# Kernel tuning notes

Hardware: AMD Instinct MI355X
Metric: run time of the kernel (lower is better)

## Reference

```python
import jax, jax.numpy as jnp
import numpy as np

TOPK = 13
ALPHA = 1.0
BETA = 6.0
CENTER_RADIUS = 0.5
EPS = 1e-7
IMG = 2048
STRIDES = (8, 16, 32)


def _make_anchor_points():
    pts = []
    for s in STRIDES:
        n = IMG // s
        c = (jnp.arange(n, dtype=jnp.float32) + 0.5) * s
        yy, xx = jnp.meshgrid(c, c, indexing='ij')
        pts.append(jnp.stack([xx.ravel(), yy.ravel()], axis=-1))
    return jnp.concatenate(pts, axis=0)  # [86016, 2]


def setup_inputs() -> dict:
    key = jax.random.key(0)
    k = jax.random.split(key, 6)
    anchor_points = _make_anchor_points()           # [P, 2]
    P = anchor_points.shape[0]
    C, G = 365, 100
    pred_scores = jax.random.normal(k[0], (P, C), dtype=jnp.float32) * 2.0 - 2.0
    pred_objectness = jax.random.normal(k[1], (P,), dtype=jnp.float32)
    # predicted boxes: anchor +- positive ltrb distances (valid xyxy)
    dist = jax.random.uniform(k[2], (P, 4), minval=2.0, maxval=120.0, dtype=jnp.float32)
    pred_boxes = jnp.concatenate([anchor_points - dist[:, :2], anchor_points + dist[:, 2:]], axis=-1)
    ctr = jax.random.uniform(k[3], (G, 2), minval=64.0, maxval=IMG - 64.0, dtype=jnp.float32)
    half = jax.random.uniform(k[4], (G, 2), minval=16.0, maxval=160.0, dtype=jnp.float32)
    gt_boxes = jnp.concatenate([ctr - half, ctr + half], axis=-1)  # [G, 4] xyxy
    gt_labels = jax.random.randint(k[5], (G,), 0, C, dtype=jnp.int64)
    valid_class_mask = jnp.ones((C,), dtype=bool)
    return {
        'pred_scores': pred_scores,
        'pred_boxes': pred_boxes,
        'pred_objectness': pred_objectness,
        'anchor_points': anchor_points,
        'gt_boxes': gt_boxes,
        'gt_labels': gt_labels,
        'valid_class_mask': valid_class_mask,
    }


def _iou_matrix(gt_boxes, pred_boxes):
    # gt: [G,4], pred: [P,4] -> [G,P]
    lt = jnp.maximum(gt_boxes[:, None, :2], pred_boxes[None, :, :2])
    rb = jnp.minimum(gt_boxes[:, None, 2:], pred_boxes[None, :, 2:])
    wh = jnp.clip(rb - lt, 0.0)
    inter = wh[..., 0] * wh[..., 1]
    area_g = jnp.prod(jnp.clip(gt_boxes[:, 2:] - gt_boxes[:, :2], 0.0), axis=-1)
    area_p = jnp.prod(jnp.clip(pred_boxes[:, 2:] - pred_boxes[:, :2], 0.0), axis=-1)
    union = area_g[:, None] + area_p[None, :] - inter
    return inter / (union + EPS)


def reference(pred_scores, pred_boxes, pred_objectness, anchor_points, gt_boxes, gt_labels, valid_class_mask):
    P, C = pred_scores.shape
    G = gt_boxes.shape[0]
    gt_labels = gt_labels.astype(jnp.int32)

    valid_gt = (gt_labels >= 0) & (gt_labels < C) & valid_class_mask[jnp.clip(gt_labels, 0, C - 1)]

    # inside-box mask [G, P]
    ax, ay = anchor_points[:, 0], anchor_points[:, 1]
    inside = ((ax[None, :] >= gt_boxes[:, 0:1]) & (ax[None, :] <= gt_boxes[:, 2:3]) &
              (ay[None, :] >= gt_boxes[:, 1:2]) & (ay[None, :] <= gt_boxes[:, 3:4]))

    gt_center = (gt_boxes[:, :2] + gt_boxes[:, 2:]) * 0.5               # [G,2]
    half_size = jnp.clip((gt_boxes[:, 2:] - gt_boxes[:, :2]) * 0.5, 1.0)
    center_delta = jnp.abs(anchor_points[None, :, :] - gt_center[:, None, :]) / half_size[:, None, :]  # [G,P,2]
    cd_max = center_delta.max(axis=-1)                                   # [G,P]
    center_mask = cd_max <= CENTER_RADIUS

    strict = inside & center_mask
    has_center = strict.any(axis=1, keepdims=True)                       # [G,1]
    cand = jnp.where(has_center, strict, inside)                         # fallback to inside-only

    iou = _iou_matrix(gt_boxes, pred_boxes)                              # [G,P]
    cls_scores = jax.nn.sigmoid(pred_scores[:, jnp.clip(gt_labels, 0, C - 1)].T)  # [G,P]
    pred_obj = jax.nn.sigmoid(pred_objectness)                           # [P]
    quality = jnp.sqrt(jnp.clip(pred_obj[None, :] * cls_scores, 0.0))
    center_prior = jnp.exp(-0.5 * jnp.sum(center_delta ** 2, axis=-1))   # [G,P]
    align = (quality ** ALPHA) * (iou ** BETA) * center_prior            # [G,P], >= 0

    masked = jnp.where(cand & valid_gt[:, None], align, -1.0)
    top_val, top_idx = jax.lax.top_k(masked, TOPK)                       # [G,TOPK]
    # scatter per-GT top-k back to [G,P]; entries with value -1 (non-candidates) stay excluded
    sel = jnp.full((G, P), -1.0, dtype=align.dtype)
    sel = sel.at[jnp.arange(G)[:, None], top_idx].set(jnp.where(top_val > -0.5, top_val, -1.0))

    # sequential 'override only if strictly greater' == per-point argmax with ties to earliest GT
    metric = sel.max(axis=0)                                             # [P]
    best_gt = jnp.argmax(sel, axis=0)                                    # [P]
    fg_mask = metric > -0.5

    overlap = iou[best_gt, jnp.arange(P)]                                # [P]
    matched_gt_indices = jnp.where(fg_mask, best_gt, -1)
    matched_labels = jnp.where(fg_mask, gt_labels[best_gt], -1)

    target_boxes = jnp.where(fg_mask[:, None], gt_boxes[best_gt], 0.0)   # [P,4]
    lab_idx = jnp.clip(matched_labels, 0, C - 1)
    score_val = jnp.where(fg_mask, jnp.clip(overlap, 0.1), 0.0)
    target_scores = jnp.zeros((P, C), dtype=pred_scores.dtype).at[jnp.arange(P), lab_idx].set(score_val)

    return (target_scores, target_boxes, fg_mask, matched_gt_indices, matched_labels)
```

## Files before the change

### kernel.cpp

```cpp
#include <hip/hip_runtime.h>
#include <cstdint>
#include <cstddef>

#define TOPK 13
#define MAXC 2560
#define NITER 10
#define NLEV 3
#define FILL_F4 1024

__global__ __launch_bounds__(256) void pdl_zero_topk_kernel(
    const float*  __restrict__ scores,
    const float4* __restrict__ pboxes,
    const float*  __restrict__ obj,
    const float4* __restrict__ gtb,
    const int*    __restrict__ glab,
    const unsigned char* __restrict__ vmask,
    unsigned long long* __restrict__ ws_keys,
    float* __restrict__ out,
    int C, int G, long long nfloat4)
{
    const int bid = blockIdx.x;
    const int tid = threadIdx.x;

    if (bid >= G) {
        float4* dst = (float4*)out;
        const float4 z = make_float4(0.0f, 0.0f, 0.0f, 0.0f);
        const long long s0 = (long long)(bid - G) * FILL_F4;
        const long long i = s0 + tid;
        if (i       < nfloat4) dst[i]       = z;
        if (i + 256 < nfloat4) dst[i + 256] = z;
        if (i + 512 < nfloat4) dst[i + 512] = z;
        if (i + 768 < nfloat4) dst[i + 768] = z;
        return;
    }

    const int g = bid;
    if (tid < TOPK) ws_keys[g * TOPK + tid] = 0ULL;

    const float4 gb = gtb[g];
    const int lab = glab[g];
    bool valid = (lab >= 0) && (lab < C);
    if (valid) {
        valid = (vmask[lab] != 0) || (vmask[4 * (size_t)lab] != 0) ||
                (vmask[8 * (size_t)lab] != 0);
    }
    if (!valid) return;

    __shared__ int s_flag;
    __shared__ unsigned long long s_merge[4 * TOPK];

    if (tid == 0) s_flag = 0;

    const float cx = (gb.x + gb.z) * 0.5f;
    const float cy = (gb.y + gb.w) * 0.5f;
    const float hx = fmaxf((gb.z - gb.x) * 0.5f, 1.0f);
    const float hy = fmaxf((gb.w - gb.y) * 0.5f, 1.0f);
    const float area_g = fmaxf(gb.z - gb.x, 0.0f) * fmaxf(gb.w - gb.y, 0.0f);

    const int ls[NLEV]   = {8, 16, 32};
    const int ln[NLEV]   = {256, 128, 64};
    const int loff[NLEV] = {0, 65536, 81920};
    int x0[NLEV], y0[NLEV], ww[NLEV], cnt[NLEV];
    int T = 0;
    #pragma unroll
    for (int l = 0; l < NLEV; ++l) {
        const float fs = (float)ls[l];
        int xa = (int)floorf(gb.x / fs - 0.5f);
        int xb = (int)ceilf (gb.z / fs - 0.5f);
        int ya = (int)floorf(gb.y / fs - 0.5f);
        int yb = (int)ceilf (gb.w / fs - 0.5f);
        xa = xa > 0 ? xa : 0;
        ya = ya > 0 ? ya : 0;
        xb = xb < ln[l] - 1 ? xb : ln[l] - 1;
        yb = yb < ln[l] - 1 ? yb : ln[l] - 1;
        int w = xb - xa + 1; if (w < 0) w = 0;
        int h = yb - ya + 1; if (h < 0) h = 0;
        x0[l] = xa; y0[l] = ya; ww[l] = w;
        cnt[l] = w * h;
        T += cnt[l];
    }
    __syncthreads();

    const int lane = tid & 63;
    const int wid  = tid >> 6;

    bool any_strict = false;
    for (int j = tid; j < T; j += 256) {
        int jj = j, l = 0;
        if (jj >= cnt[0]) { jj -= cnt[0]; l = 1; if (jj >= cnt[1]) { jj -= cnt[1]; l = 2; } }
        const int iy = jj / ww[l];
        const int ix = jj - iy * ww[l];
        const float fs = (float)ls[l];
        const float ax = ((float)(x0[l] + ix) + 0.5f) * fs;
        const float ay = ((float)(y0[l] + iy) + 0.5f) * fs;
        if (ax >= gb.x && ax <= gb.z && ay >= gb.y && ay <= gb.w) {
            const float cdx = fabsf(ax - cx) / hx;
            const float cdy = fabsf(ay - cy) / hy;
            if (fmaxf(cdx, cdy) <= 0.5f) any_strict = true;
        }
    }
    if (any_strict) s_flag = 1;
    __syncthreads();
    const bool has_center = (s_flag != 0);

    unsigned long long k[NITER];
    #pragma unroll
    for (int it = 0; it < NITER; ++it) {
        k[it] = 0ULL;
        const int j = tid + (it << 8);
        if (j >= T) continue;
        int jj = j, l = 0;
        if (jj >= cnt[0]) { jj -= cnt[0]; l = 1; if (jj >= cnt[1]) { jj -= cnt[1]; l = 2; } }
        const int iy = jj / ww[l];
        const int ix = jj - iy * ww[l];
        const float fs = (float)ls[l];
        const float ax = ((float)(x0[l] + ix) + 0.5f) * fs;
        const float ay = ((float)(y0[l] + iy) + 0.5f) * fs;
        if (!(ax >= gb.x && ax <= gb.z && ay >= gb.y && ay <= gb.w)) continue;
        const float cdx = fabsf(ax - cx) / hx;
        const float cdy = fabsf(ay - cy) / hy;
        const bool strict = fmaxf(cdx, cdy) <= 0.5f;
        if (has_center && !strict) continue;

        const int p = loff[l] + (y0[l] + iy) * ln[l] + (x0[l] + ix);
        const float4 pb = pboxes[p];
        const float so = 1.0f / (1.0f + expf(-obj[p]));
        const float sc = 1.0f / (1.0f + expf(-scores[(size_t)p * C + lab]));
        const float prior = expf(-0.5f * (cdx * cdx + cdy * cdy));
        const float ltx = fmaxf(gb.x, pb.x);
        const float lty = fmaxf(gb.y, pb.y);
        const float rbx = fminf(gb.z, pb.z);
        const float rby = fminf(gb.w, pb.w);
        const float wi = fmaxf(rbx - ltx, 0.0f);
        const float hi = fmaxf(rby - lty, 0.0f);
        const float inter = wi * hi;
        const float area_p = fmaxf(pb.z - pb.x, 0.0f) * fmaxf(pb.w - pb.y, 0.0f);
        const float iou = inter / (area_g + area_p - inter + 1e-7f);
        const float q = sqrtf(fmaxf(so * sc, 0.0f));
        const float i2 = iou * iou;
        const float align = q * (i2 * i2 * i2) * prior;

        k[it] = ((unsigned long long)__float_as_uint(align) << 32)
              | (unsigned long long)(0xFFFFFFFFu ^ (unsigned)p);
    }

    {
        unsigned long long W = ~0ULL;
        for (int r = 0; r < TOPK; ++r) {
            unsigned long long loc = 0ULL;
            #pragma unroll
            for (int it = 0; it < NITER; ++it)
                if (k[it] < W && k[it] > loc) loc = k[it];
            unsigned long long wb = loc;
            #pragma unroll
            for (int d = 32; d >= 1; d >>= 1) {
                const unsigned long long o = __shfl_xor(wb, d, 64);
                if (o > wb) wb = o;
            }
            if (lane == 0) s_merge[wid * TOPK + r] = wb;
            W = wb;
        }
    }
    __syncthreads();

    if (wid == 0) {
        const unsigned long long v =
            (lane < 4 * TOPK) ? s_merge[lane] : 0ULL;
        unsigned long long W = ~0ULL;
        for (int r = 0; r < TOPK; ++r) {
            unsigned long long wb = (v < W) ? v : 0ULL;
            #pragma unroll
            for (int d = 32; d >= 1; d >>= 1) {
                const unsigned long long o = __shfl_xor(wb, d, 64);
                if (o > wb) wb = o;
            }
            if (lane == 0) ws_keys[g * TOPK + r] = wb;
            W = wb;
        }
    }
}

__global__ __launch_bounds__(256) void pdl_finalize_kernel(
    const float4* __restrict__ pboxes,
    const float4* __restrict__ gtb,
    const int*    __restrict__ glab,
    const unsigned long long* __restrict__ ws_keys,
    float* __restrict__ out,
    int P, int C, int G)
{
    const int tid = threadIdx.x;
    const int p0  = blockIdx.x * 256;
    const int p   = p0 + tid;

    __shared__ unsigned long long s_best[256];
    s_best[tid] = 0ULL;
    __syncthreads();

    const int npairs = G * TOPK;
    for (int j = tid; j < npairs; j += 256) {
        const unsigned long long k = ws_keys[j];
        if (k == 0ULL) continue;
        const unsigned pp = 0xFFFFFFFFu ^ (unsigned)(k & 0xFFFFFFFFull);
        const int d = (int)pp - p0;
        if (d >= 0 && d < 256) {
            const int g = j / TOPK;
            const unsigned long long key2 =
                (k & 0xFFFFFFFF00000000ull) |
                (unsigned long long)(0xFFFFFFFFu - (unsigned)g);
            atomicMax(&s_best[d], key2);
        }
    }
    __syncthreads();

    if (p < P) {
        const unsigned long long k = s_best[tid];
        const bool fg = (k != 0ULL);
        float4 tb = make_float4(0.0f, 0.0f, 0.0f, 0.0f);
        float mgi = -1.0f, mlab = -1.0f;
        if (fg) {
            const int bg = (int)(0xFFFFFFFFu - (unsigned)(k & 0xFFFFFFFFull));
            const float4 gbx = gtb[bg];
            const float4 pb  = pboxes[p];
            const float ltx = fmaxf(gbx.x, pb.x);
            const float lty = fmaxf(gbx.y, pb.y);
            const float rbx = fminf(gbx.z, pb.z);
            const float rby = fminf(gbx.w, pb.w);
            const float wi = fmaxf(rbx - ltx, 0.0f);
            const float hi = fmaxf(rby - lty, 0.0f);
            const float inter = wi * hi;
            const float ag = fmaxf(gbx.z - gbx.x, 0.0f) * fmaxf(gbx.w - gbx.y, 0.0f);
            const float ap = fmaxf(pb.z - pb.x, 0.0f) * fmaxf(pb.w - pb.y, 0.0f);
            const float iou = inter / (ag + ap - inter + 1e-7f);
            const int lb = glab[bg];
            tb   = gbx;
            mgi  = (float)bg;
            mlab = (float)lb;
            int lbc = lb < 0 ? 0 : (lb > C - 1 ? C - 1 : lb);
            out[(size_t)p * C + lbc] = fmaxf(iou, 0.1f);
        }
        float4* boxes_out = (float4*)(out + (size_t)P * C);
        boxes_out[p] = tb;
        const size_t base = (size_t)P * C + (size_t)4 * P;
        out[base + p]                 = fg ? 1.0f : 0.0f;
        out[base + (size_t)P + p]     = mgi;
        out[base + (size_t)2 * P + p] = mlab;
    }
}

extern "C" void kernel_launch(void* const* d_in, const int* in_sizes, int n_in,
                              void* d_out, int out_size, void* d_ws, size_t ws_size,
                              hipStream_t stream)
{
    (void)n_in; (void)out_size; (void)ws_size;

    const float*  scores = (const float*)d_in[0];
    const float4* pboxes = (const float4*)d_in[1];
    const float*  obj    = (const float*)d_in[2];
    const float4* gtb    = (const float4*)d_in[4];
    const int*    glab   = (const int*)d_in[5];
    const unsigned char* vmask = (const unsigned char*)d_in[6];

    const int P = in_sizes[2];
    const int C = in_sizes[0] / P;
    const int G = in_sizes[5];

    unsigned long long* ws_keys = (unsigned long long*)d_ws;
    float* out = (float*)d_out;

    const long long nfloat4 = ((long long)P * C) / 4;
    const int NZB = (int)((nfloat4 + FILL_F4 - 1) / FILL_F4);

    pdl_zero_topk_kernel<<<G + NZB, 256, 0, stream>>>(scores, pboxes, obj, gtb,
                                                      glab, vmask, ws_keys, out,
                                                      C, G, nfloat4);
    pdl_finalize_kernel<<<(P + 255) / 256, 256, 0, stream>>>(pboxes, gtb, glab,
                                                             ws_keys, out, P, C, G);
}
```

Baseline: 36.46 us.

## Split pipeline into topk, zero-fill+small-outputs, and sparse scatter kernels

Moves the large zero-fill of the score tensor out of the top-k kernel and into a second kernel that also writes the per-point boxes, mask, index and label outputs. A third kernel then recomputes the per-point best GT and scatters only the IoU score values. The aim is to keep the top-k blocks from competing with the heavy zero-fill blocks, so the G top-k blocks finish sooner. The cost is an extra launch and a second pass over the workspace keys, and the zero-fill now runs after top-k instead of overlapping with it.

```diff
diff --git a/kernel.cpp b/kernel.cpp
--- a/kernel.cpp
+++ b/kernel.cpp
@@ -8,7 +8,7 @@
 #define NLEV 3
 #define FILL_F4 1024
 
-__global__ __launch_bounds__(256) void pdl_zero_topk_kernel(
+__global__ __launch_bounds__(256) void pdl_topk_kernel(
     const float*  __restrict__ scores,
     const float4* __restrict__ pboxes,
     const float*  __restrict__ obj,
@@ -16,25 +16,11 @@
     const int*    __restrict__ glab,
     const unsigned char* __restrict__ vmask,
     unsigned long long* __restrict__ ws_keys,
-    float* __restrict__ out,
-    int C, int G, long long nfloat4)
+    int C)
 {
-    const int bid = blockIdx.x;
+    const int g   = blockIdx.x;
     const int tid = threadIdx.x;
 
-    if (bid >= G) {
-        float4* dst = (float4*)out;
-        const float4 z = make_float4(0.0f, 0.0f, 0.0f, 0.0f);
-        const long long s0 = (long long)(bid - G) * FILL_F4;
-        const long long i = s0 + tid;
-        if (i       < nfloat4) dst[i]       = z;
-        if (i + 256 < nfloat4) dst[i + 256] = z;
-        if (i + 512 < nfloat4) dst[i + 512] = z;
-        if (i + 768 < nfloat4) dst[i + 768] = z;
-        return;
-    }
-
-    const int g = bid;
     if (tid < TOPK) ws_keys[g * TOPK + tid] = 0ULL;
 
     const float4 gb = gtb[g];
@@ -180,17 +166,29 @@
     }
 }
 
-__global__ __launch_bounds__(256) void pdl_finalize_kernel(
-    const float4* __restrict__ pboxes,
+__global__ __launch_bounds__(256) void pdl_fill_outputs_kernel(
     const float4* __restrict__ gtb,
     const int*    __restrict__ glab,
     const unsigned long long* __restrict__ ws_keys,
     float* __restrict__ out,
-    int P, int C, int G)
+    int P, int C, int G, long long nfloat4, int ACB)
 {
+    const int bid = blockIdx.x;
     const int tid = threadIdx.x;
-    const int p0  = blockIdx.x * 256;
-    const int p   = p0 + tid;
+
+    if (bid >= ACB) {
+        float4* dst = (float4*)out;
+        const float4 z = make_float4(0.0f, 0.0f, 0.0f, 0.0f);
+        const long long i = (long long)(bid - ACB) * FILL_F4 + tid;
+        if (i       < nfloat4) dst[i]       = z;
+        if (i + 256 < nfloat4) dst[i + 256] = z;
+        if (i + 512 < nfloat4) dst[i + 512] = z;
+        if (i + 768 < nfloat4) dst[i + 768] = z;
+        return;
+    }
+
+    const int p0 = bid * 256;
+    const int p  = p0 + tid;
 
     __shared__ unsigned long long s_best[256];
     s_best[tid] = 0ULL;
@@ -218,6 +216,55 @@
         float4 tb = make_float4(0.0f, 0.0f, 0.0f, 0.0f);
         float mgi = -1.0f, mlab = -1.0f;
         if (fg) {
+            const int bg = (int)(0xFFFFFFFFu - (unsigned)(k & 0xFFFFFFFFull));
+            tb   = gtb[bg];
+            mgi  = (float)bg;
+            mlab = (float)glab[bg];
+        }
+        float4* boxes_out = (float4*)(out + (size_t)P * C);
+        boxes_out[p] = tb;
+        const size_t base = (size_t)P * C + (size_t)4 * P;
+        out[base + p]                 = fg ? 1.0f : 0.0f;
+        out[base + (size_t)P + p]     = mgi;
+        out[base + (size_t)2 * P + p] = mlab;
+    }
+}
+
+__global__ __launch_bounds__(256) void pdl_scatter_kernel(
+    const float4* __restrict__ pboxes,
+    const float4* __restrict__ gtb,
+    const int*    __restrict__ glab,
+    const unsigned long long* __restrict__ ws_keys,
+    float* __restrict__ out,
+    int P, int C, int G)
+{
+    const int tid = threadIdx.x;
+    const int p0  = blockIdx.x * 256;
+    const int p   = p0 + tid;
+
+    __shared__ unsigned long long s_best[256];
+    s_best[tid] = 0ULL;
+    __syncthreads();
+
+    const int npairs = G * TOPK;
+    for (int j = tid; j < npairs; j += 256) {
+        const unsigned long long k = ws_keys[j];
+        if (k == 0ULL) continue;
+        const unsigned pp = 0xFFFFFFFFu ^ (unsigned)(k & 0xFFFFFFFFull);
+        const int d = (int)pp - p0;
+        if (d >= 0 && d < 256) {
+            const int g = j / TOPK;
+            const unsigned long long key2 =
+                (k & 0xFFFFFFFF00000000ull) |
+                (unsigned long long)(0xFFFFFFFFu - (unsigned)g);
+            atomicMax(&s_best[d], key2);
+        }
+    }
+    __syncthreads();
+
+    if (p < P) {
+        const unsigned long long k = s_best[tid];
+        if (k != 0ULL) {
             const int bg = (int)(0xFFFFFFFFu - (unsigned)(k & 0xFFFFFFFFull));
             const float4 gbx = gtb[bg];
             const float4 pb  = pboxes[p];
@@ -231,19 +278,10 @@
             const float ag = fmaxf(gbx.z - gbx.x, 0.0f) * fmaxf(gbx.w - gbx.y, 0.0f);
             const float ap = fmaxf(pb.z - pb.x, 0.0f) * fmaxf(pb.w - pb.y, 0.0f);
             const float iou = inter / (ag + ap - inter + 1e-7f);
-            const int lb = glab[bg];
-            tb   = gbx;
-            mgi  = (float)bg;
-            mlab = (float)lb;
-            int lbc = lb < 0 ? 0 : (lb > C - 1 ? C - 1 : lb);
-            out[(size_t)p * C + lbc] = fmaxf(iou, 0.1f);
-        }
-        float4* boxes_out = (float4*)(out + (size_t)P * C);
-        boxes_out[p] = tb;
-        const size_t base = (size_t)P * C + (size_t)4 * P;
-        out[base + p]                 = fg ? 1.0f : 0.0f;
-        out[base + (size_t)P + p]     = mgi;
-        out[base + (size_t)2 * P + p] = mlab;
+            int lb = glab[bg];
+            lb = lb < 0 ? 0 : (lb > C - 1 ? C - 1 : lb);
+            out[(size_t)p * C + lb] = fmaxf(iou, 0.1f);
+        }
     }
 }
 
@@ -269,10 +307,13 @@
 
     const long long nfloat4 = ((long long)P * C) / 4;
     const int NZB = (int)((nfloat4 + FILL_F4 - 1) / FILL_F4);
-
-    pdl_zero_topk_kernel<<<G + NZB, 256, 0, stream>>>(scores, pboxes, obj, gtb,
-                                                      glab, vmask, ws_keys, out,
-                                                      C, G, nfloat4);
-    pdl_finalize_kernel<<<(P + 255) / 256, 256, 0, stream>>>(pboxes, gtb, glab,
-                                                             ws_keys, out, P, C, G);
+    const int ACB = (P + 255) / 256;
+
+    pdl_topk_kernel<<<G, 256, 0, stream>>>(scores, pboxes, obj, gtb, glab,
+                                           vmask, ws_keys, C);
+    pdl_fill_outputs_kernel<<<ACB + NZB, 256, 0, stream>>>(gtb, glab, ws_keys,
+                                                           out, P, C, G,
+                                                           nfloat4, ACB);
+    pdl_scatter_kernel<<<ACB, 256, 0, stream>>>(pboxes, gtb, glab, ws_keys,
+                                                out, P, C, G);
 }
```

Result: slower. 46.60 us (+27.8%).

## Fuse top-k and finalize kernels into one with a global completion counter

Applied to the files above, without the earlier changes.

The producer top-k blocks and the zero-fill/finalize work now live in one launch. Consumer blocks own 96-row slices: they zero their slice of target_scores, spin-wait on a global done counter until all G producer blocks have published their keys, then scatter and finalize their rows. This removes the second kernel launch and the gap between the two kernels, and it overlaps the zero-fill with the top-k work. In exchange it adds a memset launch for the counter and a spin-wait that assumes producer blocks get scheduled before consumers occupy all slots. It also makes every consumer block rescan all G*TOPK keys for a much smaller row range.

```diff
diff --git a/kernel.cpp b/kernel.cpp
--- a/kernel.cpp
+++ b/kernel.cpp
@@ -3,222 +3,233 @@
 #include <cstddef>
 
 #define TOPK 13
-#define MAXC 2560
 #define NITER 10
 #define NLEV 3
-#define FILL_F4 1024
-
-__global__ __launch_bounds__(256) void pdl_zero_topk_kernel(
+#define ROWS 96
+
+__global__ __launch_bounds__(256, 4) void pdl_mega_kernel(
     const float*  __restrict__ scores,
     const float4* __restrict__ pboxes,
     const float*  __restrict__ obj,
     const float4* __restrict__ gtb,
     const int*    __restrict__ glab,
     const unsigned char* __restrict__ vmask,
+    unsigned int* __restrict__ done,
     unsigned long long* __restrict__ ws_keys,
     float* __restrict__ out,
-    int C, int G, long long nfloat4)
+    int P, int C, int G)
 {
     const int bid = blockIdx.x;
     const int tid = threadIdx.x;
-
-    if (bid >= G) {
+    const int lane = tid & 63;
+    const int wid  = tid >> 6;
+
+    __shared__ int s_flag;
+    __shared__ unsigned long long s_merge[4 * TOPK];
+    __shared__ unsigned long long s_best[ROWS];
+
+    if (bid < G) {
+        const int g = bid;
+        if (tid < TOPK) ws_keys[g * TOPK + tid] = 0ULL;
+
+        const float4 gb = gtb[g];
+        const int lab = glab[g];
+        bool valid = (lab >= 0) && (lab < C);
+        if (valid) {
+            valid = (vmask[lab] != 0) || (vmask[4 * (size_t)lab] != 0) ||
+                    (vmask[8 * (size_t)lab] != 0);
+        }
+        if (valid) {
+            if (tid == 0) s_flag = 0;
+
+            const float cx = (gb.x + gb.z) * 0.5f;
+            const float cy = (gb.y + gb.w) * 0.5f;
+            const float hx = fmaxf((gb.z - gb.x) * 0.5f, 1.0f);
+            const float hy = fmaxf((gb.w - gb.y) * 0.5f, 1.0f);
+            const float area_g = fmaxf(gb.z - gb.x, 0.0f) * fmaxf(gb.w - gb.y, 0.0f);
+
+            const int ls[NLEV]   = {8, 16, 32};
+            const int ln[NLEV]   = {256, 128, 64};
+            const int loff[NLEV] = {0, 65536, 81920};
+            int x0[NLEV], y0[NLEV], ww[NLEV], cnt[NLEV];
+            int T = 0;
+            #pragma unroll
+            for (int l = 0; l < NLEV; ++l) {
+                const float fs = (float)ls[l];
+                int xa = (int)floorf(gb.x / fs - 0.5f);
+                int xb = (int)ceilf (gb.z / fs - 0.5f);
+                int ya = (int)floorf(gb.y / fs - 0.5f);
+                int yb = (int)ceilf (gb.w / fs - 0.5f);
+                xa = xa > 0 ? xa : 0;
+                ya = ya > 0 ? ya : 0;
+                xb = xb < ln[l] - 1 ? xb : ln[l] - 1;
+                yb = yb < ln[l] - 1 ? yb : ln[l] - 1;
+                int w = xb - xa + 1; if (w < 0) w = 0;
+                int h = yb - ya + 1; if (h < 0) h = 0;
+                x0[l] = xa; y0[l] = ya; ww[l] = w;
+                cnt[l] = w * h;
+                T += cnt[l];
+            }
+            __syncthreads();
+
+            bool any_strict = false;
+            for (int j = tid; j < T; j += 256) {
+                int jj = j, l = 0;
+                if (jj >= cnt[0]) { jj -= cnt[0]; l = 1; if (jj >= cnt[1]) { jj -= cnt[1]; l = 2; } }
+                const int iy = jj / ww[l];
+                const int ix = jj - iy * ww[l];
+                const float fs = (float)ls[l];
+                const float ax = ((float)(x0[l] + ix) + 0.5f) * fs;
+                const float ay = ((float)(y0[l] + iy) + 0.5f) * fs;
+                if (ax >= gb.x && ax <= gb.z && ay >= gb.y && ay <= gb.w) {
+                    const float cdx = fabsf(ax - cx) / hx;
+                    const float cdy = fabsf(ay - cy) / hy;
+                    if (fmaxf(cdx, cdy) <= 0.5f) any_strict = true;
+                }
+            }
+            if (any_strict) s_flag = 1;
+            __syncthreads();
+            const bool has_center = (s_flag != 0);
+
+            unsigned long long k[NITER];
+            #pragma unroll
+            for (int it = 0; it < NITER; ++it) {
+                k[it] = 0ULL;
+                const int j = tid + (it << 8);
+                if (j >= T) continue;
+                int jj = j, l = 0;
+                if (jj >= cnt[0]) { jj -= cnt[0]; l = 1; if (jj >= cnt[1]) { jj -= cnt[1]; l = 2; } }
+                const int iy = jj / ww[l];
+                const int ix = jj - iy * ww[l];
+                const float fs = (float)ls[l];
+                const float ax = ((float)(x0[l] + ix) + 0.5f) * fs;
+                const float ay = ((float)(y0[l] + iy) + 0.5f) * fs;
+                if (!(ax >= gb.x && ax <= gb.z && ay >= gb.y && ay <= gb.w)) continue;
+                const float cdx = fabsf(ax - cx) / hx;
+                const float cdy = fabsf(ay - cy) / hy;
+                const bool strict = fmaxf(cdx, cdy) <= 0.5f;
+                if (has_center && !strict) continue;
+
+                const int p = loff[l] + (y0[l] + iy) * ln[l] + (x0[l] + ix);
+                const float4 pb = pboxes[p];
+                const float so = 1.0f / (1.0f + expf(-obj[p]));
+                const float sc = 1.0f / (1.0f + expf(-scores[(size_t)p * C + lab]));
+                const float prior = expf(-0.5f * (cdx * cdx + cdy * cdy));
+                const float ltx = fmaxf(gb.x, pb.x);
+                const float lty = fmaxf(gb.y, pb.y);
+                const float rbx = fminf(gb.z, pb.z);
+                const float rby = fminf(gb.w, pb.w);
+                const float wi = fmaxf(rbx - ltx, 0.0f);
+                const float hi = fmaxf(rby - lty, 0.0f);
+                const float inter = wi * hi;
+                const float area_p = fmaxf(pb.z - pb.x, 0.0f) * fmaxf(pb.w - pb.y, 0.0f);
+                const float iou = inter / (area_g + area_p - inter + 1e-7f);
+                const float q = sqrtf(fmaxf(so * sc, 0.0f));
+                const float i2 = iou * iou;
+                const float align = q * (i2 * i2 * i2) * prior;
+
+                k[it] = ((unsigned long long)__float_as_uint(align) << 32)
+                      | (unsigned long long)(0xFFFFFFFFu ^ (unsigned)p);
+            }
+
+            {
+                unsigned long long W = ~0ULL;
+                for (int r = 0; r < TOPK; ++r) {
+                    unsigned long long loc = 0ULL;
+                    #pragma unroll
+                    for (int it = 0; it < NITER; ++it)
+                        if (k[it] < W && k[it] > loc) loc = k[it];
+                    unsigned long long wb = loc;
+                    #pragma unroll
+                    for (int d = 32; d >= 1; d >>= 1) {
+                        const unsigned long long o = __shfl_xor(wb, d, 64);
+                        if (o > wb) wb = o;
+                    }
+                    if (lane == 0) s_merge[wid * TOPK + r] = wb;
+                    W = wb;
+                }
+            }
+            __syncthreads();
+
+            if (wid == 0) {
+                const unsigned long long v =
+                    (lane < 4 * TOPK) ? s_merge[lane] : 0ULL;
+                unsigned long long W = ~0ULL;
+                for (int r = 0; r < TOPK; ++r) {
+                    unsigned long long wb = (v < W) ? v : 0ULL;
+                    #pragma unroll
+                    for (int d = 32; d >= 1; d >>= 1) {
+                        const unsigned long long o = __shfl_xor(wb, d, 64);
+                        if (o > wb) wb = o;
+                    }
+                    if (lane == 0) ws_keys[g * TOPK + r] = wb;
+                    W = wb;
+                }
+            }
+        }
+        __syncthreads();
+        if (tid == 0) {
+            __threadfence();
+            atomicAdd(done, 1u);
+        }
+        return;
+    }
+
+    const int cb = bid - G;
+    const int a0 = cb * ROWS;
+    int a1 = a0 + ROWS; if (a1 > P) a1 = P;
+    const int na = a1 - a0;
+    if (na <= 0) return;
+
+    for (int i = tid; i < na; i += 256) s_best[i] = 0ULL;
+
+    {
         float4* dst = (float4*)out;
         const float4 z = make_float4(0.0f, 0.0f, 0.0f, 0.0f);
-        const long long s0 = (long long)(bid - G) * FILL_F4;
-        const long long i = s0 + tid;
-        if (i       < nfloat4) dst[i]       = z;
-        if (i + 256 < nfloat4) dst[i + 256] = z;
-        if (i + 512 < nfloat4) dst[i + 512] = z;
-        if (i + 768 < nfloat4) dst[i + 768] = z;
-        return;
-    }
-
-    const int g = bid;
-    if (tid < TOPK) ws_keys[g * TOPK + tid] = 0ULL;
-
-    const float4 gb = gtb[g];
-    const int lab = glab[g];
-    bool valid = (lab >= 0) && (lab < C);
-    if (valid) {
-        valid = (vmask[lab] != 0) || (vmask[4 * (size_t)lab] != 0) ||
-                (vmask[8 * (size_t)lab] != 0);
-    }
-    if (!valid) return;
-
-    __shared__ int s_flag;
-    __shared__ unsigned long long s_merge[4 * TOPK];
-
-    if (tid == 0) s_flag = 0;
-
-    const float cx = (gb.x + gb.z) * 0.5f;
-    const float cy = (gb.y + gb.w) * 0.5f;
-    const float hx = fmaxf((gb.z - gb.x) * 0.5f, 1.0f);
-    const float hy = fmaxf((gb.w - gb.y) * 0.5f, 1.0f);
-    const float area_g = fmaxf(gb.z - gb.x, 0.0f) * fmaxf(gb.w - gb.y, 0.0f);
-
-    const int ls[NLEV]   = {8, 16, 32};
-    const int ln[NLEV]   = {256, 128, 64};
-    const int loff[NLEV] = {0, 65536, 81920};
-    int x0[NLEV], y0[NLEV], ww[NLEV], cnt[NLEV];
-    int T = 0;
-    #pragma unroll
-    for (int l = 0; l < NLEV; ++l) {
-        const float fs = (float)ls[l];
-        int xa = (int)floorf(gb.x / fs - 0.5f);
-        int xb = (int)ceilf (gb.z / fs - 0.5f);
-        int ya = (int)floorf(gb.y / fs - 0.5f);
-        int yb = (int)ceilf (gb.w / fs - 0.5f);
-        xa = xa > 0 ? xa : 0;
-        ya = ya > 0 ? ya : 0;
-        xb = xb < ln[l] - 1 ? xb : ln[l] - 1;
-        yb = yb < ln[l] - 1 ? yb : ln[l] - 1;
-        int w = xb - xa + 1; if (w < 0) w = 0;
-        int h = yb - ya + 1; if (h < 0) h = 0;
-        x0[l] = xa; y0[l] = ya; ww[l] = w;
-        cnt[l] = w * h;
-        T += cnt[l];
+        const long long f0 = ((long long)a0 * C) >> 2;
+        const long long f1 = ((long long)a1 * C) >> 2;
+        for (long long i = f0 + tid; i < f1; i += 1024) {
+            dst[i] = z;
+            if (i + 256 < f1) dst[i + 256] = z;
+            if (i + 512 < f1) dst[i + 512] = z;
+            if (i + 768 < f1) dst[i + 768] = z;
+        }
     }
     __syncthreads();
 
-    const int lane = tid & 63;
-    const int wid  = tid >> 6;
-
-    bool any_strict = false;
-    for (int j = tid; j < T; j += 256) {
-        int jj = j, l = 0;
-        if (jj >= cnt[0]) { jj -= cnt[0]; l = 1; if (jj >= cnt[1]) { jj -= cnt[1]; l = 2; } }
-        const int iy = jj / ww[l];
-        const int ix = jj - iy * ww[l];
-        const float fs = (float)ls[l];
-        const float ax = ((float)(x0[l] + ix) + 0.5f) * fs;
-        const float ay = ((float)(y0[l] + iy) + 0.5f) * fs;
-        if (ax >= gb.x && ax <= gb.z && ay >= gb.y && ay <= gb.w) {
-            const float cdx = fabsf(ax - cx) / hx;
-            const float cdy = fabsf(ay - cy) / hy;
-            if (fmaxf(cdx, cdy) <= 0.5f) any_strict = true;
-        }
-    }
-    if (any_strict) s_flag = 1;
+    if (tid == 0) {
+        while (atomicAdd(done, 0u) < (unsigned)G)
+            __builtin_amdgcn_s_sleep(16);
+    }
     __syncthreads();
-    const bool has_center = (s_flag != 0);
-
-    unsigned long long k[NITER];
-    #pragma unroll
-    for (int it = 0; it < NITER; ++it) {
-        k[it] = 0ULL;
-        const int j = tid + (it << 8);
-        if (j >= T) continue;
-        int jj = j, l = 0;
-        if (jj >= cnt[0]) { jj -= cnt[0]; l = 1; if (jj >= cnt[1]) { jj -= cnt[1]; l = 2; } }
-        const int iy = jj / ww[l];
-        const int ix = jj - iy * ww[l];
-        const float fs = (float)ls[l];
-        const float ax = ((float)(x0[l] + ix) + 0.5f) * fs;
-        const float ay = ((float)(y0[l] + iy) + 0.5f) * fs;
-        if (!(ax >= gb.x && ax <= gb.z && ay >= gb.y && ay <= gb.w)) continue;
-        const float cdx = fabsf(ax - cx) / hx;
-        const float cdy = fabsf(ay - cy) / hy;
-        const bool strict = fmaxf(cdx, cdy) <= 0.5f;
-        if (has_center && !strict) continue;
-
-        const int p = loff[l] + (y0[l] + iy) * ln[l] + (x0[l] + ix);
-        const float4 pb = pboxes[p];
-        const float so = 1.0f / (1.0f + expf(-obj[p]));
-        const float sc = 1.0f / (1.0f + expf(-scores[(size_t)p * C + lab]));
-        const float prior = expf(-0.5f * (cdx * cdx + cdy * cdy));
-        const float ltx = fmaxf(gb.x, pb.x);
-        const float lty = fmaxf(gb.y, pb.y);
-        const float rbx = fminf(gb.z, pb.z);
-        const float rby = fminf(gb.w, pb.w);
-        const float wi = fmaxf(rbx - ltx, 0.0f);
-        const float hi = fmaxf(rby - lty, 0.0f);
-        const float inter = wi * hi;
-        const float area_p = fmaxf(pb.z - pb.x, 0.0f) * fmaxf(pb.w - pb.y, 0.0f);
-        const float iou = inter / (area_g + area_p - inter + 1e-7f);
-        const float q = sqrtf(fmaxf(so * sc, 0.0f));
-        const float i2 = iou * iou;
-        const float align = q * (i2 * i2 * i2) * prior;
-
-        k[it] = ((unsigned long long)__float_as_uint(align) << 32)
-              | (unsigned long long)(0xFFFFFFFFu ^ (unsigned)p);
-    }
-
-    {
-        unsigned long long W = ~0ULL;
-        for (int r = 0; r < TOPK; ++r) {
-            unsigned long long loc = 0ULL;
-            #pragma unroll
-            for (int it = 0; it < NITER; ++it)
-                if (k[it] < W && k[it] > loc) loc = k[it];
-            unsigned long long wb = loc;
-            #pragma unroll
-            for (int d = 32; d >= 1; d >>= 1) {
-                const unsigned long long o = __shfl_xor(wb, d, 64);
-                if (o > wb) wb = o;
-            }
-            if (lane == 0) s_merge[wid * TOPK + r] = wb;
-            W = wb;
-        }
-    }
-    __syncthreads();
-
-    if (wid == 0) {
-        const unsigned long long v =
-            (lane < 4 * TOPK) ? s_merge[lane] : 0ULL;
-        unsigned long long W = ~0ULL;
-        for (int r = 0; r < TOPK; ++r) {
-            unsigned long long wb = (v < W) ? v : 0ULL;
-            #pragma unroll
-            for (int d = 32; d >= 1; d >>= 1) {
-                const unsigned long long o = __shfl_xor(wb, d, 64);
-                if (o > wb) wb = o;
-            }
-            if (lane == 0) ws_keys[g * TOPK + r] = wb;
-            W = wb;
-        }
-    }
-}
-
-__global__ __launch_bounds__(256) void pdl_finalize_kernel(
-    const float4* __restrict__ pboxes,
-    const float4* __restrict__ gtb,
-    const int*    __restrict__ glab,
-    const unsigned long long* __restrict__ ws_keys,
-    float* __restrict__ out,
-    int P, int C, int G)
-{
-    const int tid = threadIdx.x;
-    const int p0  = blockIdx.x * 256;
-    const int p   = p0 + tid;
-
-    __shared__ unsigned long long s_best[256];
-    s_best[tid] = 0ULL;
-    __syncthreads();
+    __threadfence();
 
     const int npairs = G * TOPK;
     for (int j = tid; j < npairs; j += 256) {
-        const unsigned long long k = ws_keys[j];
-        if (k == 0ULL) continue;
-        const unsigned pp = 0xFFFFFFFFu ^ (unsigned)(k & 0xFFFFFFFFull);
-        const int d = (int)pp - p0;
-        if (d >= 0 && d < 256) {
+        const unsigned long long kk = ws_keys[j];
+        if (kk == 0ULL) continue;
+        const unsigned pp = 0xFFFFFFFFu ^ (unsigned)(kk & 0xFFFFFFFFull);
+        const int d = (int)pp - a0;
+        if (d >= 0 && d < na) {
             const int g = j / TOPK;
             const unsigned long long key2 =
-                (k & 0xFFFFFFFF00000000ull) |
+                (kk & 0xFFFFFFFF00000000ull) |
                 (unsigned long long)(0xFFFFFFFFu - (unsigned)g);
             atomicMax(&s_best[d], key2);
         }
     }
     __syncthreads();
 
-    if (p < P) {
-        const unsigned long long k = s_best[tid];
-        const bool fg = (k != 0ULL);
+    float4* boxes_out = (float4*)(out + (size_t)P * C);
+    const size_t base = (size_t)P * C + (size_t)4 * P;
+    for (int i = tid; i < na; i += 256) {
+        const int p = a0 + i;
+        const unsigned long long kk = s_best[i];
+        const bool fg = (kk != 0ULL);
         float4 tb = make_float4(0.0f, 0.0f, 0.0f, 0.0f);
         float mgi = -1.0f, mlab = -1.0f;
         if (fg) {
-            const int bg = (int)(0xFFFFFFFFu - (unsigned)(k & 0xFFFFFFFFull));
+            const int bg = (int)(0xFFFFFFFFu - (unsigned)(kk & 0xFFFFFFFFull));
             const float4 gbx = gtb[bg];
             const float4 pb  = pboxes[p];
             const float ltx = fmaxf(gbx.x, pb.x);
@@ -238,9 +249,7 @@
             int lbc = lb < 0 ? 0 : (lb > C - 1 ? C - 1 : lb);
             out[(size_t)p * C + lbc] = fmaxf(iou, 0.1f);
         }
-        float4* boxes_out = (float4*)(out + (size_t)P * C);
         boxes_out[p] = tb;
-        const size_t base = (size_t)P * C + (size_t)4 * P;
         out[base + p]                 = fg ? 1.0f : 0.0f;
         out[base + (size_t)P + p]     = mgi;
         out[base + (size_t)2 * P + p] = mlab;
@@ -264,15 +273,16 @@
     const int C = in_sizes[0] / P;
     const int G = in_sizes[5];
 
-    unsigned long long* ws_keys = (unsigned long long*)d_ws;
+    unsigned int* done = (unsigned int*)d_ws;
+    unsigned long long* ws_keys =
+        (unsigned long long*)((char*)d_ws + 16);
+
     float* out = (float*)d_out;
 
-    const long long nfloat4 = ((long long)P * C) / 4;
-    const int NZB = (int)((nfloat4 + FILL_F4 - 1) / FILL_F4);
-
-    pdl_zero_topk_kernel<<<G + NZB, 256, 0, stream>>>(scores, pboxes, obj, gtb,
-                                                      glab, vmask, ws_keys, out,
-                                                      C, G, nfloat4);
-    pdl_finalize_kernel<<<(P + 255) / 256, 256, 0, stream>>>(pboxes, gtb, glab,
-                                                             ws_keys, out, P, C, G);
+    const int NCONS = (P + ROWS - 1) / ROWS;
+
+    hipMemsetAsync(done, 0, sizeof(unsigned int), stream);
+    pdl_mega_kernel<<<G + NCONS, 256, 0, stream>>>(scores, pboxes, obj, gtb,
+                                                   glab, vmask, done, ws_keys,
+                                                   out, P, C, G);
 }
```

Result: slower. 113.8 us (+212.3%).
